# Performance work log

Measured on AMD Instinct MI355X. Metric: run time of the kernel, lower is better.

## Reference

```python
import jax, jax.numpy as jnp
import numpy as np

H = 1024      # hidden_size
I = 4096      # expert_intermediate_size (4*H)
E = 8         # num_experts (routed)
K = 2         # num_experts_per_token
SHARED = 1    # shared experts
LB_W = 0.01   # load_balance_loss_weight
Z_W = 0.01    # router z-loss weight
INIT_STD = 0.02


def _expert_mlp(x, gate_w, up_w, down_w):
    # SwiGLU expert: down( silu(x @ gate^T) * (x @ up^T) )
    return (jax.nn.silu(x @ gate_w.T) * (x @ up_w.T)) @ down_w.T


def setup_inputs() -> dict:
    key = jax.random.key(0)
    ks = jax.random.split(key, 8)
    f32 = jnp.float32
    return {
        'hidden_states': jax.random.normal(ks[0], (2, 2048, H), f32),
        'router_w': jax.random.normal(ks[1], (E, H), f32) * INIT_STD,
        'gate_w': jax.random.normal(ks[2], (E, I, H), f32) * INIT_STD,
        'up_w': jax.random.normal(ks[3], (E, I, H), f32) * INIT_STD,
        'down_w': jax.random.normal(ks[4], (E, H, I), f32) * INIT_STD,
        'sh_gate_w': jax.random.normal(ks[5], (I, H), f32) * INIT_STD,
        'sh_up_w': jax.random.normal(ks[6], (I, H), f32) * INIT_STD,
        'sh_down_w': jax.random.normal(ks[7], (H, I), f32) * INIT_STD,
    }


def reference(hidden_states, router_w, gate_w, up_w, down_w, sh_gate_w, sh_up_w, sh_down_w):
    B, S, Hd = hidden_states.shape
    x = hidden_states.reshape(-1, Hd)            # [T, H]
    T = x.shape[0]

    # Router (identity pre-router net, no bias)
    router_logits = x @ router_w.T               # [T, E]
    router_probs = jax.nn.softmax(router_logits, axis=-1)
    routing_weights, selected_experts = jax.lax.top_k(router_probs, K)  # [T, K]
    routing_weights = routing_weights / routing_weights.sum(-1, keepdims=True)

    # Per-token per-expert combine weights: sum_k w_k * [sel_k == e]
    onehot = jax.nn.one_hot(selected_experts, E, dtype=routing_weights.dtype)  # [T, K, E]
    combine = jnp.einsum('tk,tke->te', routing_weights, onehot)               # [T, E]

    # Routed experts (fixed small loop over E experts, vectorized over tokens)
    expert_out = jnp.zeros_like(x)
    for e in range(E):
        y = _expert_mlp(x, gate_w[e], up_w[e], down_w[e])                     # [T, H]
        expert_out = expert_out + y * combine[:, e:e + 1]

    # Shared expert(s) (SHARED == 1): averaged dense expert applied to all tokens
    shared_out = _expert_mlp(x, sh_gate_w, sh_up_w, sh_down_w) / SHARED

    final = (expert_out + shared_out).reshape(B, S, Hd)

    # Aux losses
    routed_mask = (onehot.sum(1) > 0).astype(jnp.float32)                     # [T, E]
    loads = jnp.concatenate([routed_mask.sum(0),
                             jnp.full((SHARED,), float(T), jnp.float32)])     # [E+SHARED]
    loads_n = loads / loads.sum()
    ideal = 1.0 / (E + SHARED)
    load_balance_loss = jnp.mean((loads_n - ideal) ** 2)
    router_z_loss = jnp.mean(jnp.sum(router_logits ** 2, axis=-1))
    total_aux_loss = LB_W * load_balance_loss + Z_W * router_z_loss
    return final, total_aux_loss
```

## Files before the change

### kernel.cpp

```cpp
#include <hip/hip_runtime.h>


typedef unsigned short u16;
typedef unsigned int u32;

typedef short bf16x8 __attribute__((ext_vector_type(8)));
typedef float f32x4 __attribute__((ext_vector_type(4)));

#define GLD16(g, l)                                                            \
  __builtin_amdgcn_global_load_lds(                                            \
      (const __attribute__((address_space(1))) void*)(g),                      \
      (__attribute__((address_space(3))) void*)(l), 16, 0, 0)

__device__ __forceinline__ u32 rne16(float f) {
  u32 u = __float_as_uint(f);
  return (u + 0x7fffu + ((u >> 16) & 1u)) >> 16;
}
__device__ __forceinline__ u16 bf16of(float f) { return (u16)rne16(f); }
__device__ __forceinline__ u32 pk2(float lo, float hi) {
  return rne16(lo) | (rne16(hi) << 16);
}

__device__ __forceinline__ int xcd_remap_act(int lin, int nact) {
  int xcd = lin & 7, idx = lin >> 3;
  int q = nact >> 3, r = nact & 7;
  int base = xcd < r ? xcd * (q + 1) : r * (q + 1) + (xcd - r) * q;
  return base + idx;
}


__global__ void zero_meta_kernel(int* __restrict__ meta) {
  int t = threadIdx.x;
  if (t < 8) meta[t] = 0;
  if (t == 8) ((float*)(meta + 32))[0] = 0.0f;
}

__global__ void router_kernel(const float* __restrict__ x,
                              const float* __restrict__ rw,
                              u16* __restrict__ xb, int* __restrict__ tlist,
                              float* __restrict__ gwv, int* __restrict__ meta) {
  int tok = blockIdx.x;
  int lane = threadIdx.x;
  const float* xr = x + (size_t)tok * 1024;
  float acc[8] = {0.f, 0.f, 0.f, 0.f, 0.f, 0.f, 0.f, 0.f};
#pragma unroll
  for (int c = 0; c < 16; c++) {
    float xv = xr[lane + 64 * c];
    xb[(size_t)tok * 1024 + lane + 64 * c] = bf16of(xv);
#pragma unroll
    for (int e = 0; e < 8; e++) acc[e] += xv * rw[e * 1024 + lane + 64 * c];
  }
#pragma unroll
  for (int e = 0; e < 8; e++) {
    float v = acc[e];
    for (int m = 32; m > 0; m >>= 1) v += __shfl_xor(v, m, 64);
    acc[e] = v;
  }
  if (lane == 0) {
    float z = 0.f;
#pragma unroll
    for (int e = 0; e < 8; e++) z += acc[e] * acc[e];
    atomicAdd((float*)(meta + 32), z);
    int i1 = 0;
    float b1 = acc[0];
#pragma unroll
    for (int e = 1; e < 8; e++)
      if (acc[e] > b1) { b1 = acc[e]; i1 = e; }
    int i2 = -1;
    float b2 = -3.0e38f;
#pragma unroll
    for (int e = 0; e < 8; e++)
      if (e != i1 && acc[e] > b2) { b2 = acc[e]; i2 = e; }
    float w1 = 1.0f / (1.0f + __expf(b2 - b1));
    float w2 = 1.0f - w1;
    int s1 = atomicAdd(&meta[i1], 1);
    tlist[i1 * 4096 + s1] = tok;
    gwv[i1 * 4096 + s1] = w1;
    int s2 = atomicAdd(&meta[i2], 1);
    tlist[i2 * 4096 + s2] = tok;
    gwv[i2 * 4096 + s2] = w2;
  }
}

__global__ void finalize_kernel(int* __restrict__ meta, float* __restrict__ out) {
  if (threadIdx.x == 0) {
    int* basep = meta + 16;
    int base = 0;
    float lb = 0.f;
    const float invsum = 1.0f / 12288.0f;
    const float ideal = 1.0f / 9.0f;
    for (int e = 0; e < 8; e++) {
      int c = meta[e];
      int p = (c + 127) & ~127;
      meta[8 + e] = p;
      basep[e] = base;
      base += p;
      float d = (float)c * invsum - ideal;
      lb += d * d;
    }
    basep[8] = base;
    float dsh = 4096.0f * invsum - ideal;
    lb += dsh * dsh;
    lb *= (1.0f / 9.0f);
    float z = ((float*)(meta + 32))[0] * (1.0f / 4096.0f);
    out[4194304] = 0.01f * lb + 0.01f * z;
  }
}

__global__ void gather_kernel(const u16* __restrict__ xb, u16* __restrict__ Ag,
                              const int* __restrict__ tlist,
                              const int* __restrict__ meta) {
  int r = blockIdx.x;
  int t = threadIdx.x;
  const int* base = meta + 16;
  int total = base[8];
  uint4 val = make_uint4(0u, 0u, 0u, 0u);
  if (r < total) {
    int e = 0;
#pragma unroll
    for (int q = 1; q < 8; q++)
      if (r >= base[q]) e = q;
    int s = r - base[e];
    if (s < meta[e]) {
      int tok = tlist[e * 4096 + s];
      val = *((const uint4*)(xb + (size_t)tok * 1024) + t);
    }
  }
  *((uint4*)(Ag + (size_t)r * 1024) + t) = val;
}

__global__ void conv_kernel(const float* __restrict__ src, u16* __restrict__ dst,
                            int n8) {
  int i = blockIdx.x * 256 + threadIdx.x;
  if (i >= n8) return;
  const float4* s = (const float4*)src + (size_t)i * 2;
  float4 a = s[0], b = s[1];
  uint4 o;
  o.x = pk2(a.x, a.y);
  o.y = pk2(a.z, a.w);
  o.z = pk2(b.x, b.y);
  o.w = pk2(b.z, b.w);
  ((uint4*)dst)[i] = o;
}

__global__ __launch_bounds__(256, 2) void gemm1_kernel(
    const u16* __restrict__ A, const u16* __restrict__ Wg,
    const u16* __restrict__ Wu, u16* __restrict__ Hout,
    const int* __restrict__ meta, int e_lo, int e_hi) {
  __shared__ u16 sA[128 * 32];
  __shared__ u16 sBg[128 * 32];
  __shared__ u16 sBu[128 * 32];

  const int* base = (meta != nullptr) ? (meta + 16) : nullptr;
  int gx = gridDim.x;
  int nby = (meta != nullptr) ? ((base[e_hi] - base[e_lo]) >> 7) : gridDim.y;
  int nact = nby * gx;
  int lin = blockIdx.x + gx * blockIdx.y;
  if (lin >= nact) return;
  int wg = xcd_remap_act(lin, nact);
  int per = 8 * gx;
  int nfull = nby >> 3;
  int by, bx;
  if (wg < nfull * per) {
    int stripe = wg / per, ins = wg % per;
    by = stripe * 8 + (ins & 7);
    bx = ins >> 3;
  } else {
    int rem = wg - nfull * per;
    int sh = nby - nfull * 8;
    by = nfull * 8 + rem % sh;
    bx = rem / sh;
  }

  int r0, elocal;
  if (meta != nullptr) {
    r0 = base[e_lo] + by * 128;
    int e = e_lo;
#pragma unroll
    for (int q = 1; q < 8; q++)
      if (q > e_lo && q < e_hi && r0 >= base[q]) e = q;
    elocal = e - e_lo;
  } else {
    r0 = by * 128;
    elocal = 0;
  }
  int n0 = bx * 128;
  int t = threadIdx.x;

  const u16* aP = A + (size_t)(r0 + (t >> 2)) * 1024 + (t & 3) * 8;
  const u16* gP =
      Wg + (size_t)elocal * 4194304 + (size_t)(n0 + (t >> 2)) * 1024 + (t & 3) * 8;
  const u16* uP =
      Wu + (size_t)elocal * 4194304 + (size_t)(n0 + (t >> 2)) * 1024 + (t & 3) * 8;
  u16* aD = sA + t * 8;
  u16* gD = sBg + t * 8;
  u16* uD = sBu + t * 8;

  int lane = t & 63, wid = t >> 6;
  int wm = wid >> 1, wn = wid & 1;
  int l15 = lane & 15, quad = lane >> 4;
  const u16* aR = sA + (wm * 64 + l15) * 32 + quad * 8;
  const u16* gR = sBg + (wn * 64 + l15) * 32 + quad * 8;
  const u16* uR = sBu + (wn * 64 + l15) * 32 + quad * 8;

  f32x4 accg[4][4] = {};
  f32x4 accu[4][4] = {};

#pragma unroll 1
  for (int kk = 0; kk < 32; kk++) {
    if (kk) __syncthreads();
    GLD16(aP, aD);
    GLD16(aP + 64 * 1024, aD + 2048);
    GLD16(gP, gD);
    GLD16(gP + 64 * 1024, gD + 2048);
    GLD16(uP, uD);
    GLD16(uP + 64 * 1024, uD + 2048);
    aP += 32;
    gP += 32;
    uP += 32;
    __syncthreads();

    bf16x8 af[4];
#pragma unroll
    for (int i = 0; i < 4; i++) af[i] = *(const bf16x8*)(aR + i * 512);
#pragma unroll
    for (int j = 0; j < 4; j++) {
      bf16x8 bg = *(const bf16x8*)(gR + j * 512);
      bf16x8 bu = *(const bf16x8*)(uR + j * 512);
#pragma unroll
      for (int i = 0; i < 4; i++) {
        accg[i][j] =
            __builtin_amdgcn_mfma_f32_16x16x32_bf16(af[i], bg, accg[i][j], 0, 0, 0);
        accu[i][j] =
            __builtin_amdgcn_mfma_f32_16x16x32_bf16(af[i], bu, accu[i][j], 0, 0, 0);
      }
    }
  }

#pragma unroll
  for (int i = 0; i < 4; i++) {
    int row = r0 + wm * 64 + i * 16 + quad * 4;
#pragma unroll
    for (int r = 0; r < 4; r++) {
      u16* hrow = Hout + (size_t)(row + r) * 4096 + n0 + wn * 64 + l15;
#pragma unroll
      for (int j = 0; j < 4; j++) {
        float g = accg[i][j][r];
        float u = accu[i][j][r];
        float s = g / (1.0f + __expf(-g));
        hrow[j * 16] = bf16of(s * u);
      }
    }
  }
}

__global__ __launch_bounds__(256, 2) void gemm2_kernel(
    const u16* __restrict__ A, const u16* __restrict__ Wd,
    float* __restrict__ out, const int* __restrict__ meta, int e_lo, int e_hi,
    const int* __restrict__ tlist, const float* __restrict__ gwv, int ksteps) {
  __shared__ u16 sA[128 * 32];
  __shared__ u16 sB[128 * 32];

  const int* base = (meta != nullptr) ? (meta + 16) : nullptr;
  int gx = gridDim.x;
  int nby = (meta != nullptr) ? ((base[e_hi] - base[e_lo]) >> 7) : gridDim.y;
  int actz = nby * gx;
  int nact = actz * gridDim.z;
  int lin = blockIdx.x + gx * (blockIdx.y + gridDim.y * blockIdx.z);
  if (lin >= nact) return;
  int wg = xcd_remap_act(lin, nact);
  int bz = wg / actz;
  int w2 = wg - bz * actz;
  int per = 4 * gx;
  int nfull = nby >> 2;
  int by, bx;
  if (w2 < nfull * per) {
    int stripe = w2 / per, ins = w2 % per;
    by = stripe * 4 + (ins & 3);
    bx = ins >> 2;
  } else {
    int rem = w2 - nfull * per;
    int sh = nby - nfull * 4;
    by = nfull * 4 + rem % sh;
    bx = rem / sh;
  }

  int r0, e;
  if (meta != nullptr) {
    r0 = base[e_lo] + by * 128;
    e = e_lo;
#pragma unroll
    for (int q = 1; q < 8; q++)
      if (q > e_lo && q < e_hi && r0 >= base[q]) e = q;
  } else {
    r0 = by * 128;
    e = e_lo;
  }
  int elocal = e - e_lo;
  int n0 = bx * 128;
  int k0 = bz * ksteps;
  int t = threadIdx.x;

  const u16* aP =
      A + (size_t)(r0 + (t >> 2)) * 4096 + (size_t)k0 * 32 + (t & 3) * 8;
  const u16* bP = Wd + (size_t)elocal * 4194304 +
                  (size_t)(n0 + (t >> 2)) * 4096 + (size_t)k0 * 32 + (t & 3) * 8;
  u16* aD = sA + t * 8;
  u16* bD = sB + t * 8;

  int lane = t & 63, wid = t >> 6;
  int wm = wid >> 1, wn = wid & 1;
  int l15 = lane & 15, quad = lane >> 4;
  const u16* aR = sA + (wm * 64 + l15) * 32 + quad * 8;
  const u16* bR = sB + (wn * 64 + l15) * 32 + quad * 8;

  f32x4 acc[4][4] = {};

#pragma unroll 1
  for (int kk = 0; kk < ksteps; kk++) {
    if (kk) __syncthreads();
    GLD16(aP, aD);
    GLD16(aP + 64 * 4096, aD + 2048);
    GLD16(bP, bD);
    GLD16(bP + 64 * 4096, bD + 2048);
    aP += 32;
    bP += 32;
    __syncthreads();

    bf16x8 af[4];
#pragma unroll
    for (int i = 0; i < 4; i++) af[i] = *(const bf16x8*)(aR + i * 512);
#pragma unroll
    for (int j = 0; j < 4; j++) {
      bf16x8 bb = *(const bf16x8*)(bR + j * 512);
#pragma unroll
      for (int i = 0; i < 4; i++)
        acc[i][j] =
            __builtin_amdgcn_mfma_f32_16x16x32_bf16(af[i], bb, acc[i][j], 0, 0, 0);
    }
  }

  if (meta != nullptr) {
    int cnt_e = meta[e];
    int base_e = (meta + 16)[e];
#pragma unroll
    for (int i = 0; i < 4; i++) {
#pragma unroll
      for (int r = 0; r < 4; r++) {
        int s = r0 - base_e + wm * 64 + i * 16 + quad * 4 + r;
        if (s < cnt_e) {
          int tok = tlist[e * 4096 + s];
          float w = gwv[e * 4096 + s];
          float* orow = out + (size_t)tok * 1024 + n0 + wn * 64 + l15;
#pragma unroll
          for (int j = 0; j < 4; j++) unsafeAtomicAdd(orow + j * 16, w * acc[i][j][r]);
        }
      }
    }
  } else {
#pragma unroll
    for (int i = 0; i < 4; i++) {
#pragma unroll
      for (int r = 0; r < 4; r++) {
        int tok = r0 + wm * 64 + i * 16 + quad * 4 + r;
        float* orow = out + (size_t)tok * 1024 + n0 + wn * 64 + l15;
#pragma unroll
        for (int j = 0; j < 4; j++) orow[j * 16] = acc[i][j][r];
      }
    }
  }
}

extern "C" void kernel_launch(void* const* d_in, const int* in_sizes, int n_in,
                              void* d_out, int out_size, void* d_ws,
                              size_t ws_size, hipStream_t stream) {
  const float* x = (const float*)d_in[0];
  const float* rw = (const float*)d_in[1];
  const float* gw_ = (const float*)d_in[2];
  const float* uw_ = (const float*)d_in[3];
  const float* dw_ = (const float*)d_in[4];
  const float* sg = (const float*)d_in[5];
  const float* su = (const float*)d_in[6];
  const float* sd = (const float*)d_in[7];
  float* out = (float*)d_out;
  char* ws = (char*)d_ws;

  int* meta = (int*)(ws + 0);
  int* tlist = (int*)(ws + 256);
  float* gwv = (float*)(ws + 131328);
  u16* xb = (u16*)(ws + 262400);
  u16* Ag = (u16*)(ws + 8651008);
  u16* Hb = (u16*)(ws + 27525376);
  u16* Wbuf = (u16*)(ws + 103022848);

  int ne = 4;
  if (ws_size < 170131712ULL) ne = 2;
  if (ws_size < 136577280ULL) ne = 1;
  const size_t EW = 4194304;

  zero_meta_kernel<<<1, 64, 0, stream>>>(meta);
  router_kernel<<<4096, 64, 0, stream>>>(x, rw, xb, tlist, gwv, meta);
  finalize_kernel<<<1, 64, 0, stream>>>(meta, out);
  gather_kernel<<<9216, 128, 0, stream>>>(xb, Ag, tlist, meta);

  conv_kernel<<<2048, 256, 0, stream>>>(sg, Wbuf, 524288);
  conv_kernel<<<2048, 256, 0, stream>>>(su, Wbuf + EW, 524288);
  gemm1_kernel<<<dim3(32, 32), 256, 0, stream>>>(xb, Wbuf, Wbuf + EW, Hb,
                                                 nullptr, 0, 0);
  conv_kernel<<<2048, 256, 0, stream>>>(sd, Wbuf, 524288);
  gemm2_kernel<<<dim3(8, 32, 1), 256, 0, stream>>>(Hb, Wbuf, out, nullptr, 0, 0,
                                                   tlist, gwv, 128);

  for (int g = 0; g < 8; g += ne) {
    conv_kernel<<<ne * 2048, 256, 0, stream>>>(gw_ + (size_t)g * EW, Wbuf,
                                               ne * 524288);
    conv_kernel<<<ne * 2048, 256, 0, stream>>>(uw_ + (size_t)g * EW,
                                               Wbuf + (size_t)ne * EW,
                                               ne * 524288);
    gemm1_kernel<<<dim3(32, 72), 256, 0, stream>>>(
        Ag, Wbuf, Wbuf + (size_t)ne * EW, Hb, meta, g, g + ne);
  }

  int ne2 = 2 * ne;
  if (ne2 > 8) ne2 = 8;
  for (int g = 0; g < 8; g += ne2) {
    conv_kernel<<<ne2 * 2048, 256, 0, stream>>>(dw_ + (size_t)g * EW, Wbuf,
                                                ne2 * 524288);
    gemm2_kernel<<<dim3(8, 72, 2), 256, 0, stream>>>(Hb, Wbuf, out, meta, g,
                                                     g + ne2, tlist, gwv, 64);
  }
}
```

Before: 1.051 ms.

## Fuse fp32-to-bf16 weight conversion into GEMM loads and merge shared expert into grouped GEMM

Removes the separate weight conversion kernels. The GEMM kernels now read fp32 weights directly, convert them in registers with v_cvt_pk_bf16_f32, and store them to LDS. The shared expert is appended as a ninth segment of the grouped GEMMs, so only one gemm1 and one gemm2 launch remain, and the output is zeroed first so every write can use atomics. This cuts the extra read and write of the bf16 weight copies and the launch overhead. The cost is doubled global weight traffic per tile, reloaded by every row block, and loss of the async global_load_lds path for the B operand.

```diff
diff --git a/kernel.cpp b/kernel.cpp
--- a/kernel.cpp
+++ b/kernel.cpp
@@ -17,8 +17,11 @@
   return (u + 0x7fffu + ((u >> 16) & 1u)) >> 16;
 }
 __device__ __forceinline__ u16 bf16of(float f) { return (u16)rne16(f); }
-__device__ __forceinline__ u32 pk2(float lo, float hi) {
-  return rne16(lo) | (rne16(hi) << 16);
+
+__device__ __forceinline__ u32 cvt2(float lo, float hi) {
+  u32 r;
+  asm("v_cvt_pk_bf16_f32 %0, %1, %2" : "=v"(r) : "v"(lo), "v"(hi));
+  return r;
 }
 
 __device__ __forceinline__ int xcd_remap_act(int lin, int nact) {
@@ -33,6 +36,10 @@
   int t = threadIdx.x;
   if (t < 8) meta[t] = 0;
   if (t == 8) ((float*)(meta + 32))[0] = 0.0f;
+}
+
+__global__ void zero_out_kernel(float4* __restrict__ o) {
+  o[blockIdx.x * 256 + threadIdx.x] = make_float4(0.f, 0.f, 0.f, 0.f);
 }
 
 __global__ void router_kernel(const float* __restrict__ x,
@@ -92,13 +99,14 @@
     for (int e = 0; e < 8; e++) {
       int c = meta[e];
       int p = (c + 127) & ~127;
-      meta[8 + e] = p;
       basep[e] = base;
       base += p;
       float d = (float)c * invsum - ideal;
       lb += d * d;
     }
     basep[8] = base;
+    basep[9] = base + 4096;
+    meta[8] = 4096;
     float dsh = 4096.0f * invsum - ideal;
     lb += dsh * dsh;
     lb *= (1.0f / 9.0f);
@@ -129,31 +137,18 @@
   *((uint4*)(Ag + (size_t)r * 1024) + t) = val;
 }
 
-__global__ void conv_kernel(const float* __restrict__ src, u16* __restrict__ dst,
-                            int n8) {
-  int i = blockIdx.x * 256 + threadIdx.x;
-  if (i >= n8) return;
-  const float4* s = (const float4*)src + (size_t)i * 2;
-  float4 a = s[0], b = s[1];
-  uint4 o;
-  o.x = pk2(a.x, a.y);
-  o.y = pk2(a.z, a.w);
-  o.z = pk2(b.x, b.y);
-  o.w = pk2(b.z, b.w);
-  ((uint4*)dst)[i] = o;
-}
-
 __global__ __launch_bounds__(256, 2) void gemm1_kernel(
-    const u16* __restrict__ A, const u16* __restrict__ Wg,
-    const u16* __restrict__ Wu, u16* __restrict__ Hout,
-    const int* __restrict__ meta, int e_lo, int e_hi) {
+    const u16* __restrict__ Ag, const u16* __restrict__ xb,
+    const float* __restrict__ Wg, const float* __restrict__ Wu,
+    const float* __restrict__ sg, const float* __restrict__ su,
+    u16* __restrict__ Hout, const int* __restrict__ meta) {
   __shared__ u16 sA[128 * 32];
   __shared__ u16 sBg[128 * 32];
   __shared__ u16 sBu[128 * 32];
 
-  const int* base = (meta != nullptr) ? (meta + 16) : nullptr;
+  const int* base = meta + 16;
   int gx = gridDim.x;
-  int nby = (meta != nullptr) ? ((base[e_hi] - base[e_lo]) >> 7) : gridDim.y;
+  int nby = base[9] >> 7;
   int nact = nby * gx;
   int lin = blockIdx.x + gx * blockIdx.y;
   if (lin >= nact) return;
@@ -172,26 +167,24 @@
     bx = rem / sh;
   }
 
-  int r0, elocal;
-  if (meta != nullptr) {
-    r0 = base[e_lo] + by * 128;
-    int e = e_lo;
-#pragma unroll
-    for (int q = 1; q < 8; q++)
-      if (q > e_lo && q < e_hi && r0 >= base[q]) e = q;
-    elocal = e - e_lo;
-  } else {
-    r0 = by * 128;
-    elocal = 0;
-  }
+  int r0 = by * 128;
+  int e = 0;
+#pragma unroll
+  for (int q = 1; q <= 8; q++)
+    if (r0 >= base[q]) e = q;
+
+  const u16* Asrc =
+      (e == 8) ? (xb + ((size_t)(r0 - base[8]) << 10)) : (Ag + ((size_t)r0 << 10));
+  const float* gw = (e == 8) ? sg : (Wg + (size_t)e * 4194304);
+  const float* uw = (e == 8) ? su : (Wu + (size_t)e * 4194304);
+
   int n0 = bx * 128;
   int t = threadIdx.x;
-
-  const u16* aP = A + (size_t)(r0 + (t >> 2)) * 1024 + (t & 3) * 8;
-  const u16* gP =
-      Wg + (size_t)elocal * 4194304 + (size_t)(n0 + (t >> 2)) * 1024 + (t & 3) * 8;
-  const u16* uP =
-      Wu + (size_t)elocal * 4194304 + (size_t)(n0 + (t >> 2)) * 1024 + (t & 3) * 8;
+  int trow = t >> 2, tcol = (t & 3) * 8;
+
+  const u16* aP = Asrc + (size_t)trow * 1024 + tcol;
+  const float* gP = gw + (size_t)(n0 + trow) * 1024 + tcol;
+  const float* uP = uw + (size_t)(n0 + trow) * 1024 + tcol;
   u16* aD = sA + t * 8;
   u16* gD = sBg + t * 8;
   u16* uD = sBu + t * 8;
@@ -210,11 +203,28 @@
   for (int kk = 0; kk < 32; kk++) {
     if (kk) __syncthreads();
     GLD16(aP, aD);
-    GLD16(aP + 64 * 1024, aD + 2048);
-    GLD16(gP, gD);
-    GLD16(gP + 64 * 1024, gD + 2048);
-    GLD16(uP, uD);
-    GLD16(uP + 64 * 1024, uD + 2048);
+    GLD16(aP + 65536, aD + 2048);
+    float4 g0 = *(const float4*)gP;
+    float4 g1 = *(const float4*)(gP + 4);
+    float4 g2 = *(const float4*)(gP + 65536);
+    float4 g3 = *(const float4*)(gP + 65540);
+    float4 u0 = *(const float4*)uP;
+    float4 u1 = *(const float4*)(uP + 4);
+    float4 u2 = *(const float4*)(uP + 65536);
+    float4 u3 = *(const float4*)(uP + 65540);
+    uint4 w0, w1;
+    w0.x = cvt2(g0.x, g0.y); w0.y = cvt2(g0.z, g0.w);
+    w0.z = cvt2(g1.x, g1.y); w0.w = cvt2(g1.z, g1.w);
+    w1.x = cvt2(g2.x, g2.y); w1.y = cvt2(g2.z, g2.w);
+    w1.z = cvt2(g3.x, g3.y); w1.w = cvt2(g3.z, g3.w);
+    *(uint4*)gD = w0;
+    *(uint4*)(gD + 2048) = w1;
+    w0.x = cvt2(u0.x, u0.y); w0.y = cvt2(u0.z, u0.w);
+    w0.z = cvt2(u1.x, u1.y); w0.w = cvt2(u1.z, u1.w);
+    w1.x = cvt2(u2.x, u2.y); w1.y = cvt2(u2.z, u2.w);
+    w1.z = cvt2(u3.x, u3.y); w1.w = cvt2(u3.z, u3.w);
+    *(uint4*)uD = w0;
+    *(uint4*)(uD + 2048) = w1;
     aP += 32;
     gP += 32;
     uP += 32;
@@ -254,18 +264,19 @@
   }
 }
 
-__global__ __launch_bounds__(256, 2) void gemm2_kernel(
-    const u16* __restrict__ A, const u16* __restrict__ Wd,
-    float* __restrict__ out, const int* __restrict__ meta, int e_lo, int e_hi,
-    const int* __restrict__ tlist, const float* __restrict__ gwv, int ksteps) {
+__global__ __launch_bounds__(256, 3) void gemm2_kernel(
+    const u16* __restrict__ A, const float* __restrict__ Wd,
+    const float* __restrict__ sd, float* __restrict__ out,
+    const int* __restrict__ meta, const int* __restrict__ tlist,
+    const float* __restrict__ gwv) {
   __shared__ u16 sA[128 * 32];
   __shared__ u16 sB[128 * 32];
 
-  const int* base = (meta != nullptr) ? (meta + 16) : nullptr;
+  const int* base = meta + 16;
   int gx = gridDim.x;
-  int nby = (meta != nullptr) ? ((base[e_hi] - base[e_lo]) >> 7) : gridDim.y;
+  int nby = base[9] >> 7;
   int actz = nby * gx;
-  int nact = actz * gridDim.z;
+  int nact = actz * 2;
   int lin = blockIdx.x + gx * (blockIdx.y + gridDim.y * blockIdx.z);
   if (lin >= nact) return;
   int wg = xcd_remap_act(lin, nact);
@@ -285,26 +296,20 @@
     bx = rem / sh;
   }
 
-  int r0, e;
-  if (meta != nullptr) {
-    r0 = base[e_lo] + by * 128;
-    e = e_lo;
-#pragma unroll
-    for (int q = 1; q < 8; q++)
-      if (q > e_lo && q < e_hi && r0 >= base[q]) e = q;
-  } else {
-    r0 = by * 128;
-    e = e_lo;
-  }
-  int elocal = e - e_lo;
+  int r0 = by * 128;
+  int e = 0;
+#pragma unroll
+  for (int q = 1; q <= 8; q++)
+    if (r0 >= base[q]) e = q;
+  const float* dwp = (e == 8) ? sd : (Wd + (size_t)e * 4194304);
+
   int n0 = bx * 128;
-  int k0 = bz * ksteps;
+  int k0 = bz * 2048;
   int t = threadIdx.x;
-
-  const u16* aP =
-      A + (size_t)(r0 + (t >> 2)) * 4096 + (size_t)k0 * 32 + (t & 3) * 8;
-  const u16* bP = Wd + (size_t)elocal * 4194304 +
-                  (size_t)(n0 + (t >> 2)) * 4096 + (size_t)k0 * 32 + (t & 3) * 8;
+  int trow = t >> 2, tcol = (t & 3) * 8;
+
+  const u16* aP = A + (size_t)(r0 + trow) * 4096 + k0 + tcol;
+  const float* bP = dwp + (size_t)(n0 + trow) * 4096 + k0 + tcol;
   u16* aD = sA + t * 8;
   u16* bD = sB + t * 8;
 
@@ -317,12 +322,21 @@
   f32x4 acc[4][4] = {};
 
 #pragma unroll 1
-  for (int kk = 0; kk < ksteps; kk++) {
+  for (int kk = 0; kk < 64; kk++) {
     if (kk) __syncthreads();
     GLD16(aP, aD);
-    GLD16(aP + 64 * 4096, aD + 2048);
-    GLD16(bP, bD);
-    GLD16(bP + 64 * 4096, bD + 2048);
+    GLD16(aP + 262144, aD + 2048);
+    float4 c0 = *(const float4*)bP;
+    float4 c1 = *(const float4*)(bP + 4);
+    float4 c2 = *(const float4*)(bP + 262144);
+    float4 c3 = *(const float4*)(bP + 262148);
+    uint4 w0, w1;
+    w0.x = cvt2(c0.x, c0.y); w0.y = cvt2(c0.z, c0.w);
+    w0.z = cvt2(c1.x, c1.y); w0.w = cvt2(c1.z, c1.w);
+    w1.x = cvt2(c2.x, c2.y); w1.y = cvt2(c2.z, c2.w);
+    w1.z = cvt2(c3.x, c3.y); w1.w = cvt2(c3.z, c3.w);
+    *(uint4*)bD = w0;
+    *(uint4*)(bD + 2048) = w1;
     aP += 32;
     bP += 32;
     __syncthreads();
@@ -340,32 +354,26 @@
     }
   }
 
-  if (meta != nullptr) {
-    int cnt_e = meta[e];
-    int base_e = (meta + 16)[e];
-#pragma unroll
-    for (int i = 0; i < 4; i++) {
-#pragma unroll
-      for (int r = 0; r < 4; r++) {
-        int s = r0 - base_e + wm * 64 + i * 16 + quad * 4 + r;
-        if (s < cnt_e) {
-          int tok = tlist[e * 4096 + s];
-          float w = gwv[e * 4096 + s];
-          float* orow = out + (size_t)tok * 1024 + n0 + wn * 64 + l15;
-#pragma unroll
-          for (int j = 0; j < 4; j++) unsafeAtomicAdd(orow + j * 16, w * acc[i][j][r]);
+  int cnt_e = meta[e];
+  int base_e = base[e];
+#pragma unroll
+  for (int i = 0; i < 4; i++) {
+#pragma unroll
+    for (int r = 0; r < 4; r++) {
+      int s = r0 - base_e + wm * 64 + i * 16 + quad * 4 + r;
+      if (s < cnt_e) {
+        int tok;
+        float w;
+        if (e == 8) {
+          tok = s;
+          w = 1.0f;
+        } else {
+          tok = tlist[e * 4096 + s];
+          w = gwv[e * 4096 + s];
         }
-      }
-    }
-  } else {
-#pragma unroll
-    for (int i = 0; i < 4; i++) {
-#pragma unroll
-      for (int r = 0; r < 4; r++) {
-        int tok = r0 + wm * 64 + i * 16 + quad * 4 + r;
         float* orow = out + (size_t)tok * 1024 + n0 + wn * 64 + l15;
 #pragma unroll
-        for (int j = 0; j < 4; j++) orow[j * 16] = acc[i][j][r];
+        for (int j = 0; j < 4; j++) unsafeAtomicAdd(orow + j * 16, w * acc[i][j][r]);
       }
     }
   }
@@ -391,42 +399,15 @@
   u16* xb = (u16*)(ws + 262400);
   u16* Ag = (u16*)(ws + 8651008);
   u16* Hb = (u16*)(ws + 27525376);
-  u16* Wbuf = (u16*)(ws + 103022848);
-
-  int ne = 4;
-  if (ws_size < 170131712ULL) ne = 2;
-  if (ws_size < 136577280ULL) ne = 1;
-  const size_t EW = 4194304;
 
   zero_meta_kernel<<<1, 64, 0, stream>>>(meta);
   router_kernel<<<4096, 64, 0, stream>>>(x, rw, xb, tlist, gwv, meta);
   finalize_kernel<<<1, 64, 0, stream>>>(meta, out);
   gather_kernel<<<9216, 128, 0, stream>>>(xb, Ag, tlist, meta);
-
-  conv_kernel<<<2048, 256, 0, stream>>>(sg, Wbuf, 524288);
-  conv_kernel<<<2048, 256, 0, stream>>>(su, Wbuf + EW, 524288);
-  gemm1_kernel<<<dim3(32, 32), 256, 0, stream>>>(xb, Wbuf, Wbuf + EW, Hb,
-                                                 nullptr, 0, 0);
-  conv_kernel<<<2048, 256, 0, stream>>>(sd, Wbuf, 524288);
-  gemm2_kernel<<<dim3(8, 32, 1), 256, 0, stream>>>(Hb, Wbuf, out, nullptr, 0, 0,
-                                                   tlist, gwv, 128);
-
-  for (int g = 0; g < 8; g += ne) {
-    conv_kernel<<<ne * 2048, 256, 0, stream>>>(gw_ + (size_t)g * EW, Wbuf,
-                                               ne * 524288);
-    conv_kernel<<<ne * 2048, 256, 0, stream>>>(uw_ + (size_t)g * EW,
-                                               Wbuf + (size_t)ne * EW,
-                                               ne * 524288);
-    gemm1_kernel<<<dim3(32, 72), 256, 0, stream>>>(
-        Ag, Wbuf, Wbuf + (size_t)ne * EW, Hb, meta, g, g + ne);
-  }
-
-  int ne2 = 2 * ne;
-  if (ne2 > 8) ne2 = 8;
-  for (int g = 0; g < 8; g += ne2) {
-    conv_kernel<<<ne2 * 2048, 256, 0, stream>>>(dw_ + (size_t)g * EW, Wbuf,
-                                                ne2 * 524288);
-    gemm2_kernel<<<dim3(8, 72, 2), 256, 0, stream>>>(Hb, Wbuf, out, meta, g,
-                                                     g + ne2, tlist, gwv, 64);
-  }
-}
+  zero_out_kernel<<<4096, 256, 0, stream>>>((float4*)out);
+
+  gemm1_kernel<<<dim3(32, 104), 256, 0, stream>>>(Ag, xb, gw_, uw_, sg, su, Hb,
+                                                  meta);
+  gemm2_kernel<<<dim3(8, 104, 2), 256, 0, stream>>>(Hb, dw_, sd, out, meta,
+                                                    tlist, gwv);
+}
```

After: 1.088 ms. 3.6% more time.
